# Performance work log

Hardware: AMD Instinct MI355X
Metric: run time of the kernel (lower is better)

## Reference

```python
import jax, jax.numpy as jnp
import numpy as np

B, N, D, H, L = 16, 512, 256, 8, 4
DK = D // H
EPS_LN = 1e-6
EPS_ADJ = 1e-6
NEG_INF = -1e12
LAM_ATT, LAM_DIST, LAM_ADJ = 0.3, 0.3, 0.4
SLOPE = 0.1  # leaky_relu_slope


def setup_inputs() -> dict:
    key = jax.random.key(0)
    ks = jax.random.split(key, 24)
    s = 1.0 / np.sqrt(D)
    w = lambda k: jax.random.normal(k, (L, D, D), jnp.float32) * s
    b = lambda k: jax.random.normal(k, (L, D), jnp.float32) * 0.01
    return {
        "x": jax.random.normal(ks[0], (B, N, D), jnp.float32),
        "mask": jax.random.randint(ks[1], (B, N), 0, 2, jnp.int32),
        "adj_matrix": jax.random.uniform(ks[2], (B, N, N), jnp.float32),
        "distance_matrix": jax.random.uniform(ks[3], (B, N, N), jnp.float32) * 10.0,
        "edges_att": jnp.zeros((1,), jnp.float32),  # unused (use_edge_features=False)
        "Wq": w(ks[4]), "bq": b(ks[5]),
        "Wk": w(ks[6]), "bk": b(ks[7]),
        "Wv": w(ks[8]), "bv": b(ks[9]),
        "Wo": w(ks[10]), "bo": b(ks[11]),
        "Wf1": w(ks[12]), "bf1": b(ks[13]),
        "Wf2": w(ks[14]), "bf2": b(ks[15]),
        "ln1_a": jnp.ones((L, D), jnp.float32), "ln1_b": jnp.zeros((L, D), jnp.float32),
        "ln2_a": jnp.ones((L, D), jnp.float32), "ln2_b": jnp.zeros((L, D), jnp.float32),
        "lnf_a": jnp.ones((D,), jnp.float32), "lnf_b": jnp.zeros((D,), jnp.float32),
    }


def _layernorm(x, a, b):
    # torch LayerNorm here uses unbiased std and divides by (std + eps)
    m = x.mean(-1, keepdims=True)
    s = jnp.std(x, axis=-1, ddof=1, keepdims=True)
    return a * (x - m) / (s + EPS_LN) + b


def reference(x, mask, adj_matrix, distance_matrix, edges_att,
              Wq, bq, Wk, bk, Wv, bv, Wo, bo, Wf1, bf1, Wf2, bf2,
              ln1_a, ln1_b, ln2_a, ln2_b, lnf_a, lnf_b):
    maskk = (mask != 0)[:, None, :]                      # [B,1,N] key mask
    # distance kernel: softmax(-dist) with masked keys -> weight 0
    p_dist = jax.nn.softmax(jnp.where(maskk, -distance_matrix, -jnp.inf), axis=-1)  # [B,N,N]
    # row-normalized adjacency
    p_adj = adj_matrix / (adj_matrix.sum(-1, keepdims=True) + EPS_ADJ)              # [B,N,N]
    mk4 = maskk[:, :, None, :]                           # [B,1,1,N]
    inv_sqrt_dk = 1.0 / np.sqrt(DK)

    for i in range(L):
        # --- self-attention sublayer (pre-norm residual) ---
        h_in = _layernorm(x, ln1_a[i], ln1_b[i])
        q = (h_in @ Wq[i] + bq[i]).reshape(B, N, H, DK).transpose(0, 2, 1, 3)
        k = (h_in @ Wk[i] + bk[i]).reshape(B, N, H, DK).transpose(0, 2, 1, 3)
        v = (h_in @ Wv[i] + bv[i]).reshape(B, N, H, DK).transpose(0, 2, 1, 3)
        scores = jnp.einsum('bhqd,bhkd->bhqk', q, k) * inv_sqrt_dk
        p_attn = jax.nn.softmax(jnp.where(mk4, scores, NEG_INF), axis=-1)
        # three-way fused weighting over [B,H,N,N]
        p = LAM_ATT * p_attn + LAM_DIST * p_dist[:, None] + LAM_ADJ * p_adj[:, None]
        att = jnp.einsum('bhqk,bhkd->bhqd', p, v).transpose(0, 2, 1, 3).reshape(B, N, D)
        x = x + (att @ Wo[i] + bo[i])
        # --- FFN sublayer (pre-norm residual), N_dense=2 with leaky_relu ---
        h2 = _layernorm(x, ln2_a[i], ln2_b[i])
        h2 = jax.nn.leaky_relu(h2 @ Wf1[i] + bf1[i], negative_slope=SLOPE)
        h2 = jax.nn.leaky_relu(h2 @ Wf2[i] + bf2[i], negative_slope=SLOPE)
        x = x + h2

    return _layernorm(x, lnf_a, lnf_b)
```

## Files before the change

### kernel.cpp

```cpp
#include <hip/hip_runtime.h>
#include <hip/hip_bf16.h>
#include <math.h>

constexpr int kB  = 16;
constexpr int kN  = 512;
constexpr int kD  = 256;
constexpr int kH  = 8;
constexpr int kDK = 32;
constexpr int kL  = 4;

using bf16 = __hip_bfloat16;
using short8 = __attribute__((ext_vector_type(8))) short;
using floatx4 = __attribute__((ext_vector_type(4))) float;

__device__ __forceinline__ float fast_exp2(float x) {
#if __has_builtin(__builtin_amdgcn_exp2f)
    return __builtin_amdgcn_exp2f(x);
#else
    return __expf(x * 0.69314718055994531f);
#endif
}

__device__ __forceinline__ void gl2lds16(const bf16* g, bf16* s) {
    __builtin_amdgcn_global_load_lds(
        (const __attribute__((address_space(1))) void*)g,
        (__attribute__((address_space(3))) void*)s, 16, 0, 0);
}

__device__ __forceinline__ int swzA(int row, int inrow_byte) {
    return row * 512 + (inrow_byte ^ ((row & 7) << 4));
}

__device__ __forceinline__ float blockReduceSum(float v, float* sh) {
    #pragma unroll
    for (int o = 32; o > 0; o >>= 1) v += __shfl_down(v, o, 64);
    int lane = threadIdx.x & 63, w = threadIdx.x >> 6;
    __syncthreads();
    if (lane == 0) sh[w] = v;
    __syncthreads();
    return sh[0] + sh[1] + sh[2] + sh[3];
}

__device__ __forceinline__ float blockReduceMax(float v, float* sh) {
    #pragma unroll
    for (int o = 32; o > 0; o >>= 1) v = fmaxf(v, __shfl_down(v, o, 64));
    int lane = threadIdx.x & 63, w = threadIdx.x >> 6;
    __syncthreads();
    if (lane == 0) sh[w] = v;
    __syncthreads();
    return fmaxf(fmaxf(sh[0], sh[1]), fmaxf(sh[2], sh[3]));
}

__global__ __launch_bounds__(256) void wconv_kernel(const float* __restrict__ Wq,
                                                    const float* __restrict__ Wk,
                                                    const float* __restrict__ Wv,
                                                    const float* __restrict__ Wo,
                                                    const float* __restrict__ Wf1,
                                                    const float* __restrict__ Wf2,
                                                    bf16* __restrict__ wqkv,
                                                    bf16* __restrict__ wo,
                                                    bf16* __restrict__ wf1,
                                                    bf16* __restrict__ wf2) {
    __shared__ float tile[32][33];
    int bid = blockIdx.x;
    int mat = bid >> 6;
    int t6 = bid & 63;
    int tr = t6 >> 3, tc = t6 & 7;
    int layer = mat / 6, slot = mat % 6;
    const float* src =
        slot == 0 ? Wq : slot == 1 ? Wk : slot == 2 ? Wv :
        slot == 3 ? Wo : slot == 4 ? Wf1 : Wf2;
    src += (size_t)layer * kD * kD;
    bf16* dst;
    if (slot < 3) dst = wqkv + ((size_t)layer * 768 + slot * 256) * kD;
    else dst = (slot == 3 ? wo : slot == 4 ? wf1 : wf2) + (size_t)layer * kD * kD;
    int t = threadIdx.x;
    int r = t >> 5, c = t & 31;
    #pragma unroll
    for (int i = 0; i < 4; i++)
        tile[r + i * 8][c] = src[(size_t)(tr * 32 + r + i * 8) * kD + tc * 32 + c];
    __syncthreads();
    #pragma unroll
    for (int i = 0; i < 4; i++)
        dst[(size_t)(tc * 32 + r + i * 8) * kD + tr * 32 + c] = bf16(tile[c][r + i * 8]);
}

__global__ __launch_bounds__(256) void bcat_kernel(const float* __restrict__ bq,
                                                   const float* __restrict__ bk,
                                                   const float* __restrict__ bv,
                                                   float* __restrict__ bcat) {
    int idx = blockIdx.x * 256 + threadIdx.x;
    int layer = idx / 768, j = idx % 768;
    const float* s = j < 256 ? bq : j < 512 ? bk : bv;
    bcat[idx] = s[layer * 256 + (j & 255)];
}

__global__ __launch_bounds__(256) void pc_kernel(const float* __restrict__ adj,
                                                 const float* __restrict__ dist,
                                                 const int* __restrict__ mask,
                                                 bf16* __restrict__ pcb) {
    __shared__ float sh[4];
    int row = blockIdx.x;
    int b = row >> 9;
    int t = threadIdx.x;
    const float* dr = dist + (size_t)row * kN;
    const float* ar = adj + (size_t)row * kN;
    const int* mr = mask + b * kN;
    float d0 = dr[t], d1 = dr[t + 256];
    float a0 = ar[t], a1 = ar[t + 256];
    int m0 = mr[t], m1 = mr[t + 256];
    const float kLog2e = 1.4426950408889634f;
    float s0 = m0 ? -d0 * kLog2e : -INFINITY;
    float s1 = m1 ? -d1 * kLog2e : -INFINITY;
    float mx = blockReduceMax(fmaxf(s0, s1), sh);
    float e0 = fast_exp2(s0 - mx);
    float e1 = fast_exp2(s1 - mx);
    float sum  = blockReduceSum(e0 + e1, sh);
    float asum = blockReduceSum(a0 + a1, sh);
    float w_d = 0.3f / sum;
    float w_a = 0.4f / (asum + 1e-6f);
    bf16* pr = pcb + (size_t)row * kN;
    pr[t]       = bf16(e0 * w_d + a0 * w_a);
    pr[t + 256] = bf16(e1 * w_d + a1 * w_a);
}

__global__ __launch_bounds__(256) void ln_kernel(const float* __restrict__ x,
                                                 const float* __restrict__ ga,
                                                 const float* __restrict__ gb,
                                                 bf16* __restrict__ y) {
    __shared__ float sh[4];
    int row = blockIdx.x, t = threadIdx.x;
    float v = x[(size_t)row * kD + t];
    float m = blockReduceSum(v, sh) * (1.0f / kD);
    float dd = v - m;
    float var = blockReduceSum(dd * dd, sh) * (1.0f / (kD - 1));
    float s = sqrtf(var);
    y[(size_t)row * kD + t] = bf16(ga[t] * dd / (s + 1e-6f) + gb[t]);
}

__global__ __launch_bounds__(256) void gemm_qkv(const bf16* __restrict__ A,
                                                const bf16* __restrict__ Wt,
                                                const float* __restrict__ bias,
                                                bf16* __restrict__ Cv) {
    __shared__ __align__(16) bf16 As[2][128][32];
    __shared__ __align__(16) bf16 Bs[2][64][32];
    int t = threadIdx.x;
    int m0 = blockIdx.x * 128, n0 = blockIdx.y * 64;
    int lane = t & 63, w = t >> 6, g = lane >> 4, li = lane & 15;
    int sr = lane >> 2;
    int sc = (lane & 3) * 8;

    const bf16* aSrc0 = A + (size_t)(m0 + w * 32 + sr) * kD + sc;
    const bf16* aSrc1 = aSrc0 + (size_t)16 * kD;
    const bf16* bSrc  = Wt + (size_t)(n0 + w * 16 + sr) * kD + sc;

    floatx4 zero = {0.f, 0.f, 0.f, 0.f};
    floatx4 acc[2][4];
    #pragma unroll
    for (int i = 0; i < 2; i++)
        #pragma unroll
        for (int j = 0; j < 4; j++) acc[i][j] = zero;

    auto stage = [&](int buf, int k0) {
        gl2lds16(aSrc0 + k0, &As[buf][w * 32][0]);
        gl2lds16(aSrc1 + k0, &As[buf][w * 32 + 16][0]);
        gl2lds16(bSrc  + k0, &Bs[buf][w * 16][0]);
    };

    stage(0, 0);
    __syncthreads();

    #pragma unroll
    for (int ks = 0; ks < 8; ks++) {
        const int cur = ks & 1;
        if (ks < 7) stage(cur ^ 1, (ks + 1) * 32);
        short8 af0 = *(const short8*)&As[cur][w * 32 + li][g * 8];
        short8 af1 = *(const short8*)&As[cur][w * 32 + 16 + li][g * 8];
        #pragma unroll
        for (int ct = 0; ct < 4; ct++) {
            short8 bfr = *(const short8*)&Bs[cur][ct * 16 + li][g * 8];
            acc[0][ct] = __builtin_amdgcn_mfma_f32_16x16x32_bf16(af0, bfr, acc[0][ct], 0, 0, 0);
            acc[1][ct] = __builtin_amdgcn_mfma_f32_16x16x32_bf16(af1, bfr, acc[1][ct], 0, 0, 0);
        }
        if (ks < 7) __syncthreads();
    }

    #pragma unroll
    for (int rt = 0; rt < 2; rt++) {
        #pragma unroll
        for (int ct = 0; ct < 4; ct++) {
            #pragma unroll
            for (int rr = 0; rr < 4; rr++) {
                int m = m0 + w * 32 + rt * 16 + g * 4 + rr;
                int n = n0 + ct * 16 + li;
                float v = acc[rt][ct][rr] + bias[n];
                int j = n >> 8, nn = n & 255;
                int b = m >> 9, nr = m & 511;
                int hh = nn >> 5, dk = nn & 31;
                Cv[(size_t)j * (kB * kN * kD) +
                   (((size_t)(b * kH + hh)) * kN + nr) * kDK + dk] = bf16(v);
            }
        }
    }
}

__device__ __forceinline__ void gemm_phase32(const char* asb, const bf16* __restrict__ Wt,
                                             bf16 (*Bs)[256][32],
                                             int w, int lane, int g, int li,
                                             floatx4 acc[2][4]) {
    auto stageB = [&](int buf, int k0) {
        #pragma unroll
        for (int c = 0; c < 4; c++) {
            int row = w * 64 + c * 16;
            gl2lds16(Wt + (size_t)(row + (lane >> 2)) * kD + k0 + (lane & 3) * 8,
                     &Bs[buf][row][0]);
        }
    };
    stageB(0, 0);
    __syncthreads();
    #pragma unroll
    for (int ks = 0; ks < 8; ks++) {
        const int cur = ks & 1;
        if (ks < 7) stageB(cur ^ 1, (ks + 1) * 32);
        short8 af0 = *(const short8*)(asb + swzA(li,      (ks * 4 + g) << 4));
        short8 af1 = *(const short8*)(asb + swzA(li + 16, (ks * 4 + g) << 4));
        #pragma unroll
        for (int ct = 0; ct < 4; ct++) {
            short8 bfr = *(const short8*)&Bs[cur][w * 64 + ct * 16 + li][g * 8];
            acc[0][ct] = __builtin_amdgcn_mfma_f32_16x16x32_bf16(af0, bfr, acc[0][ct], 0, 0, 0);
            acc[1][ct] = __builtin_amdgcn_mfma_f32_16x16x32_bf16(af1, bfr, acc[1][ct], 0, 0, 0);
        }
        if (ks < 7) __syncthreads();
    }
}

__device__ __forceinline__ void row_ln_stats(floatx4 xv[2][4],
                                             float (*psumS)[32], float (*psqS)[32],
                                             int w, int g, int li,
                                             float outMean[2][4], float outInv[2][4]) {
    #pragma unroll
    for (int rt = 0; rt < 2; rt++) {
        #pragma unroll
        for (int rr = 0; rr < 4; rr++) {
            float s4 = 0.f, q4 = 0.f;
            #pragma unroll
            for (int ct = 0; ct < 4; ct++) {
                float v = xv[rt][ct][rr];
                s4 += v;
                q4 += v * v;
            }
            #pragma unroll
            for (int o = 1; o < 16; o <<= 1) {
                s4 += __shfl_xor(s4, o, 64);
                q4 += __shfl_xor(q4, o, 64);
            }
            int row = rt * 16 + g * 4 + rr;
            if (li == 0) { psumS[w][row] = s4; psqS[w][row] = q4; }
        }
    }
    __syncthreads();
    #pragma unroll
    for (int rt = 0; rt < 2; rt++) {
        #pragma unroll
        for (int rr = 0; rr < 4; rr++) {
            int row = rt * 16 + g * 4 + rr;
            float s  = psumS[0][row] + psumS[1][row] + psumS[2][row] + psumS[3][row];
            float ss = psqS[0][row]  + psqS[1][row]  + psqS[2][row]  + psqS[3][row];
            float mean = s * (1.0f / kD);
            float var = (ss - (float)kD * mean * mean) * (1.0f / (kD - 1));
            outMean[rt][rr] = mean;
            outInv[rt][rr] = 1.0f / (sqrtf(var) + 1e-6f);
        }
    }
}

__global__ __launch_bounds__(256) void oproj_ln(const bf16* __restrict__ A,
                                                const bf16* __restrict__ Wt,
                                                const float* __restrict__ bias,
                                                const float* __restrict__ resid,
                                                float* __restrict__ xcOut,
                                                bf16* __restrict__ hOut,
                                                const float* __restrict__ ga,
                                                const float* __restrict__ gb) {
    __shared__ __align__(16) bf16 As[32][256];
    __shared__ __align__(16) bf16 Bs[2][256][32];
    __shared__ float psumS[4][32], psqS[4][32];

    int t = threadIdx.x;
    int m0 = blockIdx.x * 32;
    int lane = t & 63, w = t >> 6, g = lane >> 4, li = lane & 15;

    {
        int r = t >> 3;
        int cbase = (t & 7) * 4;
        const bf16* src = A + (size_t)(m0 + r) * kD;
        char* asb = (char*)&As[0][0];
        #pragma unroll
        for (int c = 0; c < 4; c++) {
            int chunk = cbase + c;
            short8 v = *(const short8*)(src + chunk * 8);
            *(short8*)(asb + swzA(r, chunk << 4)) = v;
        }
    }

    floatx4 zero = {0.f, 0.f, 0.f, 0.f};
    floatx4 acc[2][4];
    #pragma unroll
    for (int i = 0; i < 2; i++)
        #pragma unroll
        for (int j = 0; j < 4; j++) acc[i][j] = zero;

    gemm_phase32((const char*)&As[0][0], Wt, Bs, w, lane, g, li, acc);

    #pragma unroll
    for (int rt = 0; rt < 2; rt++) {
        #pragma unroll
        for (int ct = 0; ct < 4; ct++) {
            #pragma unroll
            for (int rr = 0; rr < 4; rr++) {
                int m = m0 + rt * 16 + g * 4 + rr;
                int n = w * 64 + ct * 16 + li;
                float xv = resid[(size_t)m * kD + n] + acc[rt][ct][rr] + bias[n];
                xcOut[(size_t)m * kD + n] = xv;
                acc[rt][ct][rr] = xv;
            }
        }
    }

    float mean[2][4], inv[2][4];
    row_ln_stats(acc, psumS, psqS, w, g, li, mean, inv);

    #pragma unroll
    for (int rt = 0; rt < 2; rt++) {
        #pragma unroll
        for (int ct = 0; ct < 4; ct++) {
            #pragma unroll
            for (int rr = 0; rr < 4; rr++) {
                int m = m0 + rt * 16 + g * 4 + rr;
                int n = w * 64 + ct * 16 + li;
                float y = ga[n] * (acc[rt][ct][rr] - mean[rt][rr]) * inv[rt][rr] + gb[n];
                hOut[(size_t)m * kD + n] = bf16(y);
            }
        }
    }
}

template <bool LAST>
__global__ __launch_bounds__(256) void ffn_fused(const bf16* __restrict__ A,
                                                 const bf16* __restrict__ W1t,
                                                 const float* __restrict__ b1,
                                                 const bf16* __restrict__ W2t,
                                                 const float* __restrict__ b2,
                                                 const float* __restrict__ resid,
                                                 float* __restrict__ xcOut,
                                                 bf16* __restrict__ hOut,
                                                 float* __restrict__ fOut,
                                                 const float* __restrict__ ga,
                                                 const float* __restrict__ gb) {
    __shared__ __align__(16) bf16 As[32][256];
    __shared__ __align__(16) bf16 As2[32][256];
    __shared__ __align__(16) bf16 Bs[2][256][32];
    __shared__ float psumS[4][32], psqS[4][32];

    int t = threadIdx.x;
    int m0 = blockIdx.x * 32;
    int lane = t & 63, w = t >> 6, g = lane >> 4, li = lane & 15;

    {
        int r = t >> 3;
        int cbase = (t & 7) * 4;
        const bf16* src = A + (size_t)(m0 + r) * kD;
        char* asb = (char*)&As[0][0];
        #pragma unroll
        for (int c = 0; c < 4; c++) {
            int chunk = cbase + c;
            short8 v = *(const short8*)(src + chunk * 8);
            *(short8*)(asb + swzA(r, chunk << 4)) = v;
        }
    }

    floatx4 zero = {0.f, 0.f, 0.f, 0.f};
    floatx4 acc[2][4];
    #pragma unroll
    for (int i = 0; i < 2; i++)
        #pragma unroll
        for (int j = 0; j < 4; j++) acc[i][j] = zero;

    gemm_phase32((const char*)&As[0][0], W1t, Bs, w, lane, g, li, acc);

    {
        char* as2b = (char*)&As2[0][0];
        #pragma unroll
        for (int rt = 0; rt < 2; rt++) {
            #pragma unroll
            for (int ct = 0; ct < 4; ct++) {
                #pragma unroll
                for (int rr = 0; rr < 4; rr++) {
                    int row = rt * 16 + g * 4 + rr;
                    int col = w * 64 + ct * 16 + li;
                    float v = acc[rt][ct][rr] + b1[col];
                    v = v > 0.f ? v : 0.1f * v;
                    *(bf16*)(as2b + swzA(row, col * 2)) = bf16(v);
                }
            }
        }
    }
    __syncthreads();

    #pragma unroll
    for (int i = 0; i < 2; i++)
        #pragma unroll
        for (int j = 0; j < 4; j++) acc[i][j] = zero;

    gemm_phase32((const char*)&As2[0][0], W2t, Bs, w, lane, g, li, acc);

    #pragma unroll
    for (int rt = 0; rt < 2; rt++) {
        #pragma unroll
        for (int ct = 0; ct < 4; ct++) {
            #pragma unroll
            for (int rr = 0; rr < 4; rr++) {
                int m = m0 + rt * 16 + g * 4 + rr;
                int n = w * 64 + ct * 16 + li;
                float v = acc[rt][ct][rr] + b2[n];
                v = v > 0.f ? v : 0.1f * v;
                float xv = resid[(size_t)m * kD + n] + v;
                if (!LAST) xcOut[(size_t)m * kD + n] = xv;
                acc[rt][ct][rr] = xv;
            }
        }
    }

    float mean[2][4], inv[2][4];
    row_ln_stats(acc, psumS, psqS, w, g, li, mean, inv);

    #pragma unroll
    for (int rt = 0; rt < 2; rt++) {
        #pragma unroll
        for (int ct = 0; ct < 4; ct++) {
            #pragma unroll
            for (int rr = 0; rr < 4; rr++) {
                int m = m0 + rt * 16 + g * 4 + rr;
                int n = w * 64 + ct * 16 + li;
                float y = ga[n] * (acc[rt][ct][rr] - mean[rt][rr]) * inv[rt][rr] + gb[n];
                if (LAST) fOut[(size_t)m * kD + n] = y;
                else      hOut[(size_t)m * kD + n] = bf16(y);
            }
        }
    }
}

__global__ __launch_bounds__(256, 2) void attn_mfma(const bf16* __restrict__ qb,
                                                    const bf16* __restrict__ kb,
                                                    const bf16* __restrict__ vb,
                                                    const bf16* __restrict__ pcb,
                                                    const int* __restrict__ mask,
                                                    bf16* __restrict__ att) {
    __shared__ __align__(16) bf16 Vf[16 * 2 * 64 * 8];
    __shared__ __align__(16) bf16 Pbuf[4][16][136];

    int blk = blockIdx.x;
    int qt = blk & 7;
    int bh = blk >> 3;
    int b = bh >> 3;
    int h = bh & 7;
    int t = threadIdx.x;
    int lane = t & 63, w = t >> 6;
    int g = lane >> 4, li = lane & 15;

    {
        const float4* vsrc4 = (const float4*)(vb + (size_t)bh * kN * kDK);
        #pragma unroll
        for (int it = 0; it < 8; it++) {
            int idx = t + it * 256;
            float4 raw = vsrc4[idx];
            union { float4 f; bf16 hh[8]; } u; u.f = raw;
            int f0 = idx * 8;
            int n = f0 >> 5, dk0 = f0 & 31;
            int kt = n >> 5, j = n & 7, gsl = (n >> 3) & 3;
            #pragma unroll
            for (int e = 0; e < 8; e++) {
                int dk = dk0 + e;
                int dt = dk >> 4;
                int lsl = (gsl << 4) | (dk & 15);
                Vf[((((kt << 1) | dt) << 6) | lsl) * 8 + j] = u.hh[e];
            }
        }
    }
    __syncthreads();

    const bf16* qrow = qb + ((size_t)bh * kN + qt * 64 + w * 16 + li) * kDK + g * 8;
    short8 aQ = *(const short8*)qrow;
    const bf16* kbase = kb + (size_t)bh * kN * kDK;
    const int* mb = mask + b * kN;
    unsigned mbits = 0;
    #pragma unroll
    for (int tt = 0; tt < 32; tt++)
        mbits |= (unsigned)(mb[tt * 16 + li] != 0) << tt;

    floatx4 s[32];
    floatx4 zero = {0.f, 0.f, 0.f, 0.f};
    #pragma unroll
    for (int tt = 0; tt < 32; tt++) {
        short8 bK = *(const short8*)(kbase + (size_t)(tt * 16 + li) * kDK + g * 8);
        s[tt] = __builtin_amdgcn_mfma_f32_16x16x32_bf16(aQ, bK, zero, 0, 0, 0);
    }

    const float scale = 0.17677669529663689f * 1.4426950408889634f;
    #pragma unroll
    for (int tt = 0; tt < 32; tt++) {
        bool mm = (mbits >> tt) & 1;
        #pragma unroll
        for (int r = 0; r < 4; r++)
            s[tt][r] = mm ? s[tt][r] * scale : -1e12f;
    }

    #pragma unroll
    for (int r = 0; r < 4; r++) {
        float mx = s[0][r];
        #pragma unroll
        for (int tt = 1; tt < 32; tt++) mx = fmaxf(mx, s[tt][r]);
        #pragma unroll
        for (int o = 1; o < 16; o <<= 1) mx = fmaxf(mx, __shfl_xor(mx, o, 64));
        float sum = 0.f;
        #pragma unroll
        for (int tt = 0; tt < 32; tt++) {
            float e = fast_exp2(s[tt][r] - mx);
            s[tt][r] = e;
            sum += e;
        }
        #pragma unroll
        for (int o = 1; o < 16; o <<= 1) sum += __shfl_xor(sum, o, 64);
        float inv = 0.3f / sum;
        #pragma unroll
        for (int tt = 0; tt < 32; tt++) s[tt][r] *= inv;
    }

    bf16* pb = &Pbuf[w][0][0];
    const bf16* pcrow = pcb + ((size_t)b * kN + qt * 64 + w * 16) * kN;
    floatx4 accA0 = zero, accA1 = zero, accB0 = zero, accB1 = zero;
    #pragma unroll
    for (int c = 0; c < 4; c++) {
        #pragma unroll
        for (int ttl = 0; ttl < 8; ttl++) {
            int tt = c * 8 + ttl;
            int kcol = ttl * 16 + li;
            #pragma unroll
            for (int r = 0; r < 4; r++)
                pb[(g * 4 + r) * 136 + kcol] = bf16(s[tt][r]);
        }
        #pragma unroll
        for (int k2 = 0; k2 < 4; k2++) {
            int ktile = c * 4 + k2;
            short8 aP = *(const short8*)(pb + li * 136 + k2 * 32 + g * 8);
            short8 aC = *(const short8*)(pcrow + (size_t)li * kN + c * 128 + k2 * 32 + g * 8);
            short8 bV0 = *(const short8*)(&Vf[((ktile * 2 + 0) * 64 + lane) * 8]);
            short8 bV1 = *(const short8*)(&Vf[((ktile * 2 + 1) * 64 + lane) * 8]);
            accA0 = __builtin_amdgcn_mfma_f32_16x16x32_bf16(aP, bV0, accA0, 0, 0, 0);
            accA1 = __builtin_amdgcn_mfma_f32_16x16x32_bf16(aP, bV1, accA1, 0, 0, 0);
            accB0 = __builtin_amdgcn_mfma_f32_16x16x32_bf16(aC, bV0, accB0, 0, 0, 0);
            accB1 = __builtin_amdgcn_mfma_f32_16x16x32_bf16(aC, bV1, accB1, 0, 0, 0);
        }
    }

    #pragma unroll
    for (int r = 0; r < 4; r++) {
        size_t row = (size_t)b * kN + qt * 64 + w * 16 + g * 4 + r;
        bf16* arow = att + row * kD + h * kDK;
        arow[li]      = bf16(accA0[r] + accB0[r]);
        arow[16 + li] = bf16(accA1[r] + accB1[r]);
    }
}

extern "C" void kernel_launch(void* const* d_in, const int* in_sizes, int n_in,
                              void* d_out, int out_size, void* d_ws, size_t ws_size,
                              hipStream_t stream) {
    const float* x    = (const float*)d_in[0];
    const int*   mask = (const int*)d_in[1];
    const float* adj  = (const float*)d_in[2];
    const float* dist = (const float*)d_in[3];
    const float* Wq = (const float*)d_in[5];  const float* bq = (const float*)d_in[6];
    const float* Wk = (const float*)d_in[7];  const float* bk = (const float*)d_in[8];
    const float* Wv = (const float*)d_in[9];  const float* bv = (const float*)d_in[10];
    const float* Wo = (const float*)d_in[11]; const float* bo = (const float*)d_in[12];
    const float* Wf1 = (const float*)d_in[13]; const float* bf1 = (const float*)d_in[14];
    const float* Wf2 = (const float*)d_in[15]; const float* bf2 = (const float*)d_in[16];
    const float* ln1a = (const float*)d_in[17]; const float* ln1b = (const float*)d_in[18];
    const float* ln2a = (const float*)d_in[19]; const float* ln2b = (const float*)d_in[20];
    const float* lnfa = (const float*)d_in[21]; const float* lnfb = (const float*)d_in[22];

    const size_t rows = (size_t)kB * kN;
    const size_t actN = rows * kD;

    char* wsb = (char*)d_ws;
    bf16*  pcb   = (bf16*)wsb;  wsb += (size_t)kB * kN * kN * sizeof(bf16);
    float* xc    = (float*)wsb; wsb += actN * sizeof(float);
    bf16*  h     = (bf16*)wsb;  wsb += actN * sizeof(bf16);
    bf16*  attb  = (bf16*)wsb;  wsb += actN * sizeof(bf16);
    bf16*  qkvb  = (bf16*)wsb;  wsb += 3 * actN * sizeof(bf16);
    bf16*  wqkv  = (bf16*)wsb;  wsb += (size_t)kL * 768 * kD * sizeof(bf16);
    bf16*  wo_t  = (bf16*)wsb;  wsb += (size_t)kL * kD * kD * sizeof(bf16);
    bf16*  wf1_t = (bf16*)wsb;  wsb += (size_t)kL * kD * kD * sizeof(bf16);
    bf16*  wf2_t = (bf16*)wsb;  wsb += (size_t)kL * kD * kD * sizeof(bf16);
    float* bcat  = (float*)wsb; wsb += (size_t)kL * 768 * sizeof(float);

    wconv_kernel<<<24 * 64, 256, 0, stream>>>(Wq, Wk, Wv, Wo, Wf1, Wf2, wqkv, wo_t, wf1_t, wf2_t);
    bcat_kernel<<<kL * 768 / 256, 256, 0, stream>>>(bq, bk, bv, bcat);
    pc_kernel<<<kB * kN, 256, 0, stream>>>(adj, dist, mask, pcb);
    ln_kernel<<<rows, 256, 0, stream>>>(x, ln1a, ln1b, h);

    dim3 gQKV(64, 12);
    const int g32 = rows / 32;
    for (int i = 0; i < kL; i++) {
        const size_t bOff = (size_t)i * kD;
        const size_t wOff = (size_t)i * kD * kD;
        const float* xin = (i == 0) ? x : xc;
        gemm_qkv<<<gQKV, 256, 0, stream>>>(h, wqkv + (size_t)i * 768 * kD,
                                           bcat + (size_t)i * 768, qkvb);
        attn_mfma<<<kB * kH * (kN / 64), 256, 0, stream>>>(qkvb, qkvb + actN, qkvb + 2 * actN,
                                                           pcb, mask, attb);
        oproj_ln<<<g32, 256, 0, stream>>>(attb, wo_t + wOff, bo + bOff, xin,
                                          xc, h, ln2a + bOff, ln2b + bOff);
        if (i < kL - 1) {
            ffn_fused<false><<<g32, 256, 0, stream>>>(h, wf1_t + wOff, bf1 + bOff,
                                                      wf2_t + wOff, bf2 + bOff,
                                                      xc, xc, h, nullptr,
                                                      ln1a + (size_t)(i + 1) * kD,
                                                      ln1b + (size_t)(i + 1) * kD);
        } else {
            ffn_fused<true><<<g32, 256, 0, stream>>>(h, wf1_t + wOff, bf1 + bOff,
                                                     wf2_t + wOff, bf2 + bOff,
                                                     xc, nullptr, nullptr, (float*)d_out,
                                                     lnfa, lnfb);
        }
    }
}
```

Baseline: 396.1 us.

## Share head-independent pc@V product across heads and store V transposed

The combined distance/adjacency weight matrix is the same for every head, so its product with V is now computed once per batch as a [N,N]x[N,D] GEMM in extra blocks of the attention launch, instead of once per head inside each attention block. The QKV GEMM now writes V in a transposed per-head layout, so the attention blocks read it straight from global memory and drop the LDS V reshuffle. The two partial attention outputs are summed in bf16 when o-proj loads its input, which adds one more activation buffer read and an extra rounding step.

Result: slower. 476.4 us (+20.3%).

```diff
diff --git a/kernel.cpp b/kernel.cpp
--- a/kernel.cpp
+++ b/kernel.cpp
@@ -19,6 +19,15 @@
 #else
     return __expf(x * 0.69314718055994531f);
 #endif
+}
+
+__device__ __forceinline__ float bfs2f(short s) {
+    unsigned u = ((unsigned)(unsigned short)s) << 16;
+    return __uint_as_float(u);
+}
+__device__ __forceinline__ short f2bfs(float f) {
+    bf16 b(f);
+    return *reinterpret_cast<short*>(&b);
 }
 
 __device__ __forceinline__ void gl2lds16(const bf16* g, bf16* s) {
@@ -197,10 +206,171 @@
                 int j = n >> 8, nn = n & 255;
                 int b = m >> 9, nr = m & 511;
                 int hh = nn >> 5, dk = nn & 31;
-                Cv[(size_t)j * (kB * kN * kD) +
-                   (((size_t)(b * kH + hh)) * kN + nr) * kDK + dk] = bf16(v);
-            }
-        }
+                size_t off = (size_t)j * (kB * kN * kD);
+                if (j < 2)
+                    Cv[off + (((size_t)(b * kH + hh)) * kN + nr) * kDK + dk] = bf16(v);
+                else
+                    Cv[off + (((size_t)(b * kH + hh)) * kDK + dk) * kN + nr] = bf16(v);
+            }
+        }
+    }
+}
+
+struct SmGemm { bf16 As[2][128][32]; bf16 Bs[2][64][32]; };
+struct SmAttn { bf16 P[4][16][136]; };
+union SmU { SmGemm g; SmAttn a; };
+
+__global__ __launch_bounds__(256) void attn_pc(const bf16* __restrict__ qb,
+                                               const bf16* __restrict__ kb,
+                                               const bf16* __restrict__ vtb,
+                                               const bf16* __restrict__ pcb,
+                                               const int* __restrict__ mask,
+                                               bf16* __restrict__ att,
+                                               bf16* __restrict__ attpc) {
+    __shared__ __align__(16) SmU sm;
+    int t = threadIdx.x;
+    int lane = t & 63, w = t >> 6;
+    int g = lane >> 4, li = lane & 15;
+    floatx4 zero = {0.f, 0.f, 0.f, 0.f};
+
+    if (blockIdx.x >= 1024) {
+        int idx = blockIdx.x - 1024;
+        int b  = idx >> 4;
+        int mt = (idx >> 2) & 3, nt = idx & 3;
+        int m0 = mt * 128, n0 = nt * 64;
+        int sr = lane >> 2, sc = (lane & 3) * 8;
+
+        const bf16* Arows = pcb + ((size_t)b * kN) * kN;
+        const bf16* Brows = vtb + ((size_t)b * kD) * kN;
+        const bf16* aSrc0 = Arows + (size_t)(m0 + w * 32 + sr) * kN + sc;
+        const bf16* aSrc1 = aSrc0 + (size_t)16 * kN;
+        const bf16* bSrc  = Brows + (size_t)(n0 + w * 16 + sr) * kN + sc;
+
+        floatx4 acc[2][4];
+        #pragma unroll
+        for (int i = 0; i < 2; i++)
+            #pragma unroll
+            for (int j = 0; j < 4; j++) acc[i][j] = zero;
+
+        auto stage = [&](int buf, int k0) {
+            gl2lds16(aSrc0 + k0, &sm.g.As[buf][w * 32][0]);
+            gl2lds16(aSrc1 + k0, &sm.g.As[buf][w * 32 + 16][0]);
+            gl2lds16(bSrc  + k0, &sm.g.Bs[buf][w * 16][0]);
+        };
+        stage(0, 0);
+        __syncthreads();
+        #pragma unroll
+        for (int ks = 0; ks < 16; ks++) {
+            const int cur = ks & 1;
+            if (ks < 15) stage(cur ^ 1, (ks + 1) * 32);
+            short8 af0 = *(const short8*)&sm.g.As[cur][w * 32 + li][g * 8];
+            short8 af1 = *(const short8*)&sm.g.As[cur][w * 32 + 16 + li][g * 8];
+            #pragma unroll
+            for (int ct = 0; ct < 4; ct++) {
+                short8 bfr = *(const short8*)&sm.g.Bs[cur][ct * 16 + li][g * 8];
+                acc[0][ct] = __builtin_amdgcn_mfma_f32_16x16x32_bf16(af0, bfr, acc[0][ct], 0, 0, 0);
+                acc[1][ct] = __builtin_amdgcn_mfma_f32_16x16x32_bf16(af1, bfr, acc[1][ct], 0, 0, 0);
+            }
+            if (ks < 15) __syncthreads();
+        }
+        #pragma unroll
+        for (int rt = 0; rt < 2; rt++) {
+            #pragma unroll
+            for (int ct = 0; ct < 4; ct++) {
+                #pragma unroll
+                for (int rr = 0; rr < 4; rr++) {
+                    int m = m0 + w * 32 + rt * 16 + g * 4 + rr;
+                    int n = n0 + ct * 16 + li;
+                    attpc[((size_t)b * kN + m) * kD + n] = bf16(acc[rt][ct][rr]);
+                }
+            }
+        }
+        return;
+    }
+
+    int blk = blockIdx.x;
+    int qt = blk & 7;
+    int bh = blk >> 3;
+    int b = bh >> 3;
+    int h = bh & 7;
+
+    const bf16* qrow = qb + ((size_t)bh * kN + qt * 64 + w * 16 + li) * kDK + g * 8;
+    short8 aQ = *(const short8*)qrow;
+    const bf16* kbase = kb + (size_t)bh * kN * kDK;
+    const int* mb = mask + b * kN;
+    unsigned mbits = 0;
+    #pragma unroll
+    for (int tt = 0; tt < 32; tt++)
+        mbits |= (unsigned)(mb[tt * 16 + li] != 0) << tt;
+
+    floatx4 s[32];
+    #pragma unroll
+    for (int tt = 0; tt < 32; tt++) {
+        short8 bK = *(const short8*)(kbase + (size_t)(tt * 16 + li) * kDK + g * 8);
+        s[tt] = __builtin_amdgcn_mfma_f32_16x16x32_bf16(aQ, bK, zero, 0, 0, 0);
+    }
+
+    const float scale = 0.17677669529663689f * 1.4426950408889634f;
+    #pragma unroll
+    for (int tt = 0; tt < 32; tt++) {
+        bool mm = (mbits >> tt) & 1;
+        #pragma unroll
+        for (int r = 0; r < 4; r++)
+            s[tt][r] = mm ? s[tt][r] * scale : -1e12f;
+    }
+
+    #pragma unroll
+    for (int r = 0; r < 4; r++) {
+        float mx = s[0][r];
+        #pragma unroll
+        for (int tt = 1; tt < 32; tt++) mx = fmaxf(mx, s[tt][r]);
+        #pragma unroll
+        for (int o = 1; o < 16; o <<= 1) mx = fmaxf(mx, __shfl_xor(mx, o, 64));
+        float sum = 0.f;
+        #pragma unroll
+        for (int tt = 0; tt < 32; tt++) {
+            float e = fast_exp2(s[tt][r] - mx);
+            s[tt][r] = e;
+            sum += e;
+        }
+        #pragma unroll
+        for (int o = 1; o < 16; o <<= 1) sum += __shfl_xor(sum, o, 64);
+        float inv = 0.3f / sum;
+        #pragma unroll
+        for (int tt = 0; tt < 32; tt++) s[tt][r] *= inv;
+    }
+
+    bf16* pb = &sm.a.P[w][0][0];
+    const bf16* vrow0 = vtb + ((size_t)bh * kDK + li) * kN;
+    const bf16* vrow1 = vrow0 + (size_t)16 * kN;
+    floatx4 accA0 = zero, accA1 = zero;
+    #pragma unroll
+    for (int c = 0; c < 4; c++) {
+        #pragma unroll
+        for (int ttl = 0; ttl < 8; ttl++) {
+            int tt = c * 8 + ttl;
+            int kcol = ttl * 16 + li;
+            #pragma unroll
+            for (int r = 0; r < 4; r++)
+                pb[(g * 4 + r) * 136 + kcol] = bf16(s[tt][r]);
+        }
+        #pragma unroll
+        for (int k2 = 0; k2 < 4; k2++) {
+            int ktile = c * 4 + k2;
+            short8 aP  = *(const short8*)(pb + li * 136 + k2 * 32 + g * 8);
+            short8 bV0 = *(const short8*)(vrow0 + ktile * 32 + g * 8);
+            short8 bV1 = *(const short8*)(vrow1 + ktile * 32 + g * 8);
+            accA0 = __builtin_amdgcn_mfma_f32_16x16x32_bf16(aP, bV0, accA0, 0, 0, 0);
+            accA1 = __builtin_amdgcn_mfma_f32_16x16x32_bf16(aP, bV1, accA1, 0, 0, 0);
+        }
+    }
+
+    #pragma unroll
+    for (int r = 0; r < 4; r++) {
+        size_t row = (size_t)b * kN + qt * 64 + w * 16 + g * 4 + r;
+        bf16* arow = att + row * kD + h * kDK;
+        arow[li]      = bf16(accA0[r]);
+        arow[16 + li] = bf16(accA1[r]);
     }
 }
 
@@ -275,6 +445,7 @@
 }
 
 __global__ __launch_bounds__(256) void oproj_ln(const bf16* __restrict__ A,
+                                                const bf16* __restrict__ A2,
                                                 const bf16* __restrict__ Wt,
                                                 const float* __restrict__ bias,
                                                 const float* __restrict__ resid,
@@ -293,13 +464,18 @@
     {
         int r = t >> 3;
         int cbase = (t & 7) * 4;
-        const bf16* src = A + (size_t)(m0 + r) * kD;
+        const bf16* src  = A  + (size_t)(m0 + r) * kD;
+        const bf16* src2 = A2 + (size_t)(m0 + r) * kD;
         char* asb = (char*)&As[0][0];
         #pragma unroll
         for (int c = 0; c < 4; c++) {
             int chunk = cbase + c;
-            short8 v = *(const short8*)(src + chunk * 8);
-            *(short8*)(asb + swzA(r, chunk << 4)) = v;
+            short8 v1 = *(const short8*)(src  + chunk * 8);
+            short8 v2 = *(const short8*)(src2 + chunk * 8);
+            short8 o;
+            #pragma unroll
+            for (int e = 0; e < 8; e++) o[e] = f2bfs(bfs2f(v1[e]) + bfs2f(v2[e]));
+            *(short8*)(asb + swzA(r, chunk << 4)) = o;
         }
     }
 
@@ -450,128 +626,6 @@
     }
 }
 
-__global__ __launch_bounds__(256, 2) void attn_mfma(const bf16* __restrict__ qb,
-                                                    const bf16* __restrict__ kb,
-                                                    const bf16* __restrict__ vb,
-                                                    const bf16* __restrict__ pcb,
-                                                    const int* __restrict__ mask,
-                                                    bf16* __restrict__ att) {
-    __shared__ __align__(16) bf16 Vf[16 * 2 * 64 * 8];
-    __shared__ __align__(16) bf16 Pbuf[4][16][136];
-
-    int blk = blockIdx.x;
-    int qt = blk & 7;
-    int bh = blk >> 3;
-    int b = bh >> 3;
-    int h = bh & 7;
-    int t = threadIdx.x;
-    int lane = t & 63, w = t >> 6;
-    int g = lane >> 4, li = lane & 15;
-
-    {
-        const float4* vsrc4 = (const float4*)(vb + (size_t)bh * kN * kDK);
-        #pragma unroll
-        for (int it = 0; it < 8; it++) {
-            int idx = t + it * 256;
-            float4 raw = vsrc4[idx];
-            union { float4 f; bf16 hh[8]; } u; u.f = raw;
-            int f0 = idx * 8;
-            int n = f0 >> 5, dk0 = f0 & 31;
-            int kt = n >> 5, j = n & 7, gsl = (n >> 3) & 3;
-            #pragma unroll
-            for (int e = 0; e < 8; e++) {
-                int dk = dk0 + e;
-                int dt = dk >> 4;
-                int lsl = (gsl << 4) | (dk & 15);
-                Vf[((((kt << 1) | dt) << 6) | lsl) * 8 + j] = u.hh[e];
-            }
-        }
-    }
-    __syncthreads();
-
-    const bf16* qrow = qb + ((size_t)bh * kN + qt * 64 + w * 16 + li) * kDK + g * 8;
-    short8 aQ = *(const short8*)qrow;
-    const bf16* kbase = kb + (size_t)bh * kN * kDK;
-    const int* mb = mask + b * kN;
-    unsigned mbits = 0;
-    #pragma unroll
-    for (int tt = 0; tt < 32; tt++)
-        mbits |= (unsigned)(mb[tt * 16 + li] != 0) << tt;
-
-    floatx4 s[32];
-    floatx4 zero = {0.f, 0.f, 0.f, 0.f};
-    #pragma unroll
-    for (int tt = 0; tt < 32; tt++) {
-        short8 bK = *(const short8*)(kbase + (size_t)(tt * 16 + li) * kDK + g * 8);
-        s[tt] = __builtin_amdgcn_mfma_f32_16x16x32_bf16(aQ, bK, zero, 0, 0, 0);
-    }
-
-    const float scale = 0.17677669529663689f * 1.4426950408889634f;
-    #pragma unroll
-    for (int tt = 0; tt < 32; tt++) {
-        bool mm = (mbits >> tt) & 1;
-        #pragma unroll
-        for (int r = 0; r < 4; r++)
-            s[tt][r] = mm ? s[tt][r] * scale : -1e12f;
-    }
-
-    #pragma unroll
-    for (int r = 0; r < 4; r++) {
-        float mx = s[0][r];
-        #pragma unroll
-        for (int tt = 1; tt < 32; tt++) mx = fmaxf(mx, s[tt][r]);
-        #pragma unroll
-        for (int o = 1; o < 16; o <<= 1) mx = fmaxf(mx, __shfl_xor(mx, o, 64));
-        float sum = 0.f;
-        #pragma unroll
-        for (int tt = 0; tt < 32; tt++) {
-            float e = fast_exp2(s[tt][r] - mx);
-            s[tt][r] = e;
-            sum += e;
-        }
-        #pragma unroll
-        for (int o = 1; o < 16; o <<= 1) sum += __shfl_xor(sum, o, 64);
-        float inv = 0.3f / sum;
-        #pragma unroll
-        for (int tt = 0; tt < 32; tt++) s[tt][r] *= inv;
-    }
-
-    bf16* pb = &Pbuf[w][0][0];
-    const bf16* pcrow = pcb + ((size_t)b * kN + qt * 64 + w * 16) * kN;
-    floatx4 accA0 = zero, accA1 = zero, accB0 = zero, accB1 = zero;
-    #pragma unroll
-    for (int c = 0; c < 4; c++) {
-        #pragma unroll
-        for (int ttl = 0; ttl < 8; ttl++) {
-            int tt = c * 8 + ttl;
-            int kcol = ttl * 16 + li;
-            #pragma unroll
-            for (int r = 0; r < 4; r++)
-                pb[(g * 4 + r) * 136 + kcol] = bf16(s[tt][r]);
-        }
-        #pragma unroll
-        for (int k2 = 0; k2 < 4; k2++) {
-            int ktile = c * 4 + k2;
-            short8 aP = *(const short8*)(pb + li * 136 + k2 * 32 + g * 8);
-            short8 aC = *(const short8*)(pcrow + (size_t)li * kN + c * 128 + k2 * 32 + g * 8);
-            short8 bV0 = *(const short8*)(&Vf[((ktile * 2 + 0) * 64 + lane) * 8]);
-            short8 bV1 = *(const short8*)(&Vf[((ktile * 2 + 1) * 64 + lane) * 8]);
-            accA0 = __builtin_amdgcn_mfma_f32_16x16x32_bf16(aP, bV0, accA0, 0, 0, 0);
-            accA1 = __builtin_amdgcn_mfma_f32_16x16x32_bf16(aP, bV1, accA1, 0, 0, 0);
-            accB0 = __builtin_amdgcn_mfma_f32_16x16x32_bf16(aC, bV0, accB0, 0, 0, 0);
-            accB1 = __builtin_amdgcn_mfma_f32_16x16x32_bf16(aC, bV1, accB1, 0, 0, 0);
-        }
-    }
-
-    #pragma unroll
-    for (int r = 0; r < 4; r++) {
-        size_t row = (size_t)b * kN + qt * 64 + w * 16 + g * 4 + r;
-        bf16* arow = att + row * kD + h * kDK;
-        arow[li]      = bf16(accA0[r] + accB0[r]);
-        arow[16 + li] = bf16(accA1[r] + accB1[r]);
-    }
-}
-
 extern "C" void kernel_launch(void* const* d_in, const int* in_sizes, int n_in,
                               void* d_out, int out_size, void* d_ws, size_t ws_size,
                               hipStream_t stream) {
@@ -597,6 +651,7 @@
     float* xc    = (float*)wsb; wsb += actN * sizeof(float);
     bf16*  h     = (bf16*)wsb;  wsb += actN * sizeof(bf16);
     bf16*  attb  = (bf16*)wsb;  wsb += actN * sizeof(bf16);
+    bf16*  attb2 = (bf16*)wsb;  wsb += actN * sizeof(bf16);
     bf16*  qkvb  = (bf16*)wsb;  wsb += 3 * actN * sizeof(bf16);
     bf16*  wqkv  = (bf16*)wsb;  wsb += (size_t)kL * 768 * kD * sizeof(bf16);
     bf16*  wo_t  = (bf16*)wsb;  wsb += (size_t)kL * kD * kD * sizeof(bf16);
@@ -617,9 +672,9 @@
         const float* xin = (i == 0) ? x : xc;
         gemm_qkv<<<gQKV, 256, 0, stream>>>(h, wqkv + (size_t)i * 768 * kD,
                                            bcat + (size_t)i * 768, qkvb);
-        attn_mfma<<<kB * kH * (kN / 64), 256, 0, stream>>>(qkvb, qkvb + actN, qkvb + 2 * actN,
-                                                           pcb, mask, attb);
-        oproj_ln<<<g32, 256, 0, stream>>>(attb, wo_t + wOff, bo + bOff, xin,
+        attn_pc<<<1024 + 256, 256, 0, stream>>>(qkvb, qkvb + actN, qkvb + 2 * actN,
+                                                pcb, mask, attb, attb2);
+        oproj_ln<<<g32, 256, 0, stream>>>(attb, attb2, wo_t + wOff, bo + bOff, xin,
                                           xc, h, ln2a + bOff, ln2b + bOff);
         if (i < kL - 1) {
             ffn_fused<false><<<g32, 256, 0, stream>>>(h, wf1_t + wOff, bf1 + bOff,
```

## Write V transposed from QKV GEMM and read it directly in attention

Applied to the files above, without the earlier changes.

The QKV GEMM now stages V-column tiles through shared memory and writes V in a transposed [bh][dk][n] layout with 16-byte stores. The attention kernel drops its per-block LDS rearrangement of V and reads B-operand fragments for the PV MFMAs straight from global memory. This removes redundant V reshuffling, which was repeated for each of 8 query tiles per head, along with its LDS footprint and a barrier. The cost is extra LDS traffic and a sync in the GEMM epilogue, plus uncached global reads of V inside the attention inner loop.

Result: slower. 488.2 us (+23.2%).

```diff
diff --git a/kernel.cpp b/kernel.cpp
--- a/kernel.cpp
+++ b/kernel.cpp
@@ -142,8 +142,10 @@
                                                 const bf16* __restrict__ Wt,
                                                 const float* __restrict__ bias,
                                                 bf16* __restrict__ Cv) {
-    __shared__ __align__(16) bf16 As[2][128][32];
-    __shared__ __align__(16) bf16 Bs[2][64][32];
+    __shared__ __align__(16) union {
+        struct { bf16 As[2][128][32]; bf16 Bs[2][64][32]; } g;
+        bf16 tr[64][136];
+    } sm;
     int t = threadIdx.x;
     int m0 = blockIdx.x * 128, n0 = blockIdx.y * 64;
     int lane = t & 63, w = t >> 6, g = lane >> 4, li = lane & 15;
@@ -162,9 +164,9 @@
         for (int j = 0; j < 4; j++) acc[i][j] = zero;
 
     auto stage = [&](int buf, int k0) {
-        gl2lds16(aSrc0 + k0, &As[buf][w * 32][0]);
-        gl2lds16(aSrc1 + k0, &As[buf][w * 32 + 16][0]);
-        gl2lds16(bSrc  + k0, &Bs[buf][w * 16][0]);
+        gl2lds16(aSrc0 + k0, &sm.g.As[buf][w * 32][0]);
+        gl2lds16(aSrc1 + k0, &sm.g.As[buf][w * 32 + 16][0]);
+        gl2lds16(bSrc  + k0, &sm.g.Bs[buf][w * 16][0]);
     };
 
     stage(0, 0);
@@ -174,33 +176,165 @@
     for (int ks = 0; ks < 8; ks++) {
         const int cur = ks & 1;
         if (ks < 7) stage(cur ^ 1, (ks + 1) * 32);
-        short8 af0 = *(const short8*)&As[cur][w * 32 + li][g * 8];
-        short8 af1 = *(const short8*)&As[cur][w * 32 + 16 + li][g * 8];
+        short8 af0 = *(const short8*)&sm.g.As[cur][w * 32 + li][g * 8];
+        short8 af1 = *(const short8*)&sm.g.As[cur][w * 32 + 16 + li][g * 8];
         #pragma unroll
         for (int ct = 0; ct < 4; ct++) {
-            short8 bfr = *(const short8*)&Bs[cur][ct * 16 + li][g * 8];
+            short8 bfr = *(const short8*)&sm.g.Bs[cur][ct * 16 + li][g * 8];
             acc[0][ct] = __builtin_amdgcn_mfma_f32_16x16x32_bf16(af0, bfr, acc[0][ct], 0, 0, 0);
             acc[1][ct] = __builtin_amdgcn_mfma_f32_16x16x32_bf16(af1, bfr, acc[1][ct], 0, 0, 0);
         }
         if (ks < 7) __syncthreads();
     }
 
-    #pragma unroll
-    for (int rt = 0; rt < 2; rt++) {
-        #pragma unroll
-        for (int ct = 0; ct < 4; ct++) {
-            #pragma unroll
-            for (int rr = 0; rr < 4; rr++) {
-                int m = m0 + w * 32 + rt * 16 + g * 4 + rr;
-                int n = n0 + ct * 16 + li;
-                float v = acc[rt][ct][rr] + bias[n];
-                int j = n >> 8, nn = n & 255;
-                int b = m >> 9, nr = m & 511;
-                int hh = nn >> 5, dk = nn & 31;
-                Cv[(size_t)j * (kB * kN * kD) +
-                   (((size_t)(b * kH + hh)) * kN + nr) * kDK + dk] = bf16(v);
-            }
-        }
+    if (blockIdx.y < 8) {
+        #pragma unroll
+        for (int rt = 0; rt < 2; rt++) {
+            #pragma unroll
+            for (int ct = 0; ct < 4; ct++) {
+                #pragma unroll
+                for (int rr = 0; rr < 4; rr++) {
+                    int m = m0 + w * 32 + rt * 16 + g * 4 + rr;
+                    int n = n0 + ct * 16 + li;
+                    float v = acc[rt][ct][rr] + bias[n];
+                    int j = n >> 8, nn = n & 255;
+                    int b = m >> 9, nr = m & 511;
+                    int hh = nn >> 5, dk = nn & 31;
+                    Cv[(size_t)j * (kB * kN * kD) +
+                       (((size_t)(b * kH + hh)) * kN + nr) * kDK + dk] = bf16(v);
+                }
+            }
+        }
+    } else {
+        __syncthreads();
+        #pragma unroll
+        for (int rt = 0; rt < 2; rt++) {
+            #pragma unroll
+            for (int ct = 0; ct < 4; ct++) {
+                #pragma unroll
+                for (int rr = 0; rr < 4; rr++) {
+                    int mloc = w * 32 + rt * 16 + g * 4 + rr;
+                    int ncol = ct * 16 + li;
+                    sm.tr[ncol][mloc] = bf16(acc[rt][ct][rr] + bias[n0 + ncol]);
+                }
+            }
+        }
+        __syncthreads();
+        int b = m0 >> 9;
+        int nrbase = m0 & 511;
+        bf16* vtb = Cv + 2 * (size_t)(kB * kN * kD);
+        #pragma unroll
+        for (int it = 0; it < 4; it++) {
+            int idx = t + it * 256;
+            int rid = idx >> 4;
+            int cid = (idx & 15) * 8;
+            int nn = (n0 + rid) & 255;
+            int hh = nn >> 5, dk = nn & 31;
+            bf16* dst = vtb + (((size_t)(b * kH + hh)) * kDK + dk) * kN + nrbase + cid;
+            *(short8*)dst = *(const short8*)&sm.tr[rid][cid];
+        }
+    }
+}
+
+__global__ __launch_bounds__(256) void attn_mfma(const bf16* __restrict__ qb,
+                                                 const bf16* __restrict__ kb,
+                                                 const bf16* __restrict__ vtb,
+                                                 const bf16* __restrict__ pcb,
+                                                 const int* __restrict__ mask,
+                                                 bf16* __restrict__ att) {
+    __shared__ __align__(16) bf16 Pbuf[4][16][136];
+
+    int blk = blockIdx.x;
+    int qt = blk & 7;
+    int bh = blk >> 3;
+    int b = bh >> 3;
+    int h = bh & 7;
+    int t = threadIdx.x;
+    int lane = t & 63, w = t >> 6;
+    int g = lane >> 4, li = lane & 15;
+    floatx4 zero = {0.f, 0.f, 0.f, 0.f};
+
+    const bf16* qrow = qb + ((size_t)bh * kN + qt * 64 + w * 16 + li) * kDK + g * 8;
+    short8 aQ = *(const short8*)qrow;
+    const bf16* kbase = kb + (size_t)bh * kN * kDK;
+    const int* mb = mask + b * kN;
+    unsigned mbits = 0;
+    #pragma unroll
+    for (int tt = 0; tt < 32; tt++)
+        mbits |= (unsigned)(mb[tt * 16 + li] != 0) << tt;
+
+    floatx4 s[32];
+    #pragma unroll
+    for (int tt = 0; tt < 32; tt++) {
+        short8 bK = *(const short8*)(kbase + (size_t)(tt * 16 + li) * kDK + g * 8);
+        s[tt] = __builtin_amdgcn_mfma_f32_16x16x32_bf16(aQ, bK, zero, 0, 0, 0);
+    }
+
+    const float scale = 0.17677669529663689f * 1.4426950408889634f;
+    #pragma unroll
+    for (int tt = 0; tt < 32; tt++) {
+        bool mm = (mbits >> tt) & 1;
+        #pragma unroll
+        for (int r = 0; r < 4; r++)
+            s[tt][r] = mm ? s[tt][r] * scale : -1e12f;
+    }
+
+    #pragma unroll
+    for (int r = 0; r < 4; r++) {
+        float mx = s[0][r];
+        #pragma unroll
+        for (int tt = 1; tt < 32; tt++) mx = fmaxf(mx, s[tt][r]);
+        #pragma unroll
+        for (int o = 1; o < 16; o <<= 1) mx = fmaxf(mx, __shfl_xor(mx, o, 64));
+        float sum = 0.f;
+        #pragma unroll
+        for (int tt = 0; tt < 32; tt++) {
+            float e = fast_exp2(s[tt][r] - mx);
+            s[tt][r] = e;
+            sum += e;
+        }
+        #pragma unroll
+        for (int o = 1; o < 16; o <<= 1) sum += __shfl_xor(sum, o, 64);
+        float inv = 0.3f / sum;
+        #pragma unroll
+        for (int tt = 0; tt < 32; tt++) s[tt][r] *= inv;
+    }
+
+    bf16* pb = &Pbuf[w][0][0];
+    const bf16* pcrow = pcb + ((size_t)b * kN + qt * 64 + w * 16) * kN;
+    const bf16* vrow0 = vtb + ((size_t)bh * kDK + li) * kN;
+    const bf16* vrow1 = vrow0 + (size_t)16 * kN;
+    floatx4 accA0 = zero, accA1 = zero, accB0 = zero, accB1 = zero;
+    #pragma unroll
+    for (int c = 0; c < 4; c++) {
+        #pragma unroll
+        for (int ttl = 0; ttl < 8; ttl++) {
+            int tt = c * 8 + ttl;
+            int kcol = ttl * 16 + li;
+            #pragma unroll
+            for (int r = 0; r < 4; r++)
+                pb[(g * 4 + r) * 136 + kcol] = bf16(s[tt][r]);
+        }
+        #pragma unroll
+        for (int k2 = 0; k2 < 4; k2++) {
+            int ktile = c * 4 + k2;
+            short8 aP  = *(const short8*)(pb + li * 136 + k2 * 32 + g * 8);
+            short8 aC  = *(const short8*)(pcrow + (size_t)li * kN + c * 128 + k2 * 32 + g * 8);
+            short8 bV0 = *(const short8*)(vrow0 + ktile * 32 + g * 8);
+            short8 bV1 = *(const short8*)(vrow1 + ktile * 32 + g * 8);
+            accA0 = __builtin_amdgcn_mfma_f32_16x16x32_bf16(aP, bV0, accA0, 0, 0, 0);
+            accA1 = __builtin_amdgcn_mfma_f32_16x16x32_bf16(aP, bV1, accA1, 0, 0, 0);
+            accB0 = __builtin_amdgcn_mfma_f32_16x16x32_bf16(aC, bV0, accB0, 0, 0, 0);
+            accB1 = __builtin_amdgcn_mfma_f32_16x16x32_bf16(aC, bV1, accB1, 0, 0, 0);
+        }
+    }
+
+    #pragma unroll
+    for (int r = 0; r < 4; r++) {
+        size_t row = (size_t)b * kN + qt * 64 + w * 16 + g * 4 + r;
+        bf16* arow = att + row * kD + h * kDK;
+        arow[li]      = bf16(accA0[r] + accB0[r]);
+        arow[16 + li] = bf16(accA1[r] + accB1[r]);
     }
 }
 
@@ -450,128 +584,6 @@
     }
 }
 
-__global__ __launch_bounds__(256, 2) void attn_mfma(const bf16* __restrict__ qb,
-                                                    const bf16* __restrict__ kb,
-                                                    const bf16* __restrict__ vb,
-                                                    const bf16* __restrict__ pcb,
-                                                    const int* __restrict__ mask,
-                                                    bf16* __restrict__ att) {
-    __shared__ __align__(16) bf16 Vf[16 * 2 * 64 * 8];
-    __shared__ __align__(16) bf16 Pbuf[4][16][136];
-
-    int blk = blockIdx.x;
-    int qt = blk & 7;
-    int bh = blk >> 3;
-    int b = bh >> 3;
-    int h = bh & 7;
-    int t = threadIdx.x;
-    int lane = t & 63, w = t >> 6;
-    int g = lane >> 4, li = lane & 15;
-
-    {
-        const float4* vsrc4 = (const float4*)(vb + (size_t)bh * kN * kDK);
-        #pragma unroll
-        for (int it = 0; it < 8; it++) {
-            int idx = t + it * 256;
-            float4 raw = vsrc4[idx];
-            union { float4 f; bf16 hh[8]; } u; u.f = raw;
-            int f0 = idx * 8;
-            int n = f0 >> 5, dk0 = f0 & 31;
-            int kt = n >> 5, j = n & 7, gsl = (n >> 3) & 3;
-            #pragma unroll
-            for (int e = 0; e < 8; e++) {
-                int dk = dk0 + e;
-                int dt = dk >> 4;
-                int lsl = (gsl << 4) | (dk & 15);
-                Vf[((((kt << 1) | dt) << 6) | lsl) * 8 + j] = u.hh[e];
-            }
-        }
-    }
-    __syncthreads();
-
-    const bf16* qrow = qb + ((size_t)bh * kN + qt * 64 + w * 16 + li) * kDK + g * 8;
-    short8 aQ = *(const short8*)qrow;
-    const bf16* kbase = kb + (size_t)bh * kN * kDK;
-    const int* mb = mask + b * kN;
-    unsigned mbits = 0;
-    #pragma unroll
-    for (int tt = 0; tt < 32; tt++)
-        mbits |= (unsigned)(mb[tt * 16 + li] != 0) << tt;
-
-    floatx4 s[32];
-    floatx4 zero = {0.f, 0.f, 0.f, 0.f};
-    #pragma unroll
-    for (int tt = 0; tt < 32; tt++) {
-        short8 bK = *(const short8*)(kbase + (size_t)(tt * 16 + li) * kDK + g * 8);
-        s[tt] = __builtin_amdgcn_mfma_f32_16x16x32_bf16(aQ, bK, zero, 0, 0, 0);
-    }
-
-    const float scale = 0.17677669529663689f * 1.4426950408889634f;
-    #pragma unroll
-    for (int tt = 0; tt < 32; tt++) {
-        bool mm = (mbits >> tt) & 1;
-        #pragma unroll
-        for (int r = 0; r < 4; r++)
-            s[tt][r] = mm ? s[tt][r] * scale : -1e12f;
-    }
-
-    #pragma unroll
-    for (int r = 0; r < 4; r++) {
-        float mx = s[0][r];
-        #pragma unroll
-        for (int tt = 1; tt < 32; tt++) mx = fmaxf(mx, s[tt][r]);
-        #pragma unroll
-        for (int o = 1; o < 16; o <<= 1) mx = fmaxf(mx, __shfl_xor(mx, o, 64));
-        float sum = 0.f;
-        #pragma unroll
-        for (int tt = 0; tt < 32; tt++) {
-            float e = fast_exp2(s[tt][r] - mx);
-            s[tt][r] = e;
-            sum += e;
-        }
-        #pragma unroll
-        for (int o = 1; o < 16; o <<= 1) sum += __shfl_xor(sum, o, 64);
-        float inv = 0.3f / sum;
-        #pragma unroll
-        for (int tt = 0; tt < 32; tt++) s[tt][r] *= inv;
-    }
-
-    bf16* pb = &Pbuf[w][0][0];
-    const bf16* pcrow = pcb + ((size_t)b * kN + qt * 64 + w * 16) * kN;
-    floatx4 accA0 = zero, accA1 = zero, accB0 = zero, accB1 = zero;
-    #pragma unroll
-    for (int c = 0; c < 4; c++) {
-        #pragma unroll
-        for (int ttl = 0; ttl < 8; ttl++) {
-            int tt = c * 8 + ttl;
-            int kcol = ttl * 16 + li;
-            #pragma unroll
-            for (int r = 0; r < 4; r++)
-                pb[(g * 4 + r) * 136 + kcol] = bf16(s[tt][r]);
-        }
-        #pragma unroll
-        for (int k2 = 0; k2 < 4; k2++) {
-            int ktile = c * 4 + k2;
-            short8 aP = *(const short8*)(pb + li * 136 + k2 * 32 + g * 8);
-            short8 aC = *(const short8*)(pcrow + (size_t)li * kN + c * 128 + k2 * 32 + g * 8);
-            short8 bV0 = *(const short8*)(&Vf[((ktile * 2 + 0) * 64 + lane) * 8]);
-            short8 bV1 = *(const short8*)(&Vf[((ktile * 2 + 1) * 64 + lane) * 8]);
-            accA0 = __builtin_amdgcn_mfma_f32_16x16x32_bf16(aP, bV0, accA0, 0, 0, 0);
-            accA1 = __builtin_amdgcn_mfma_f32_16x16x32_bf16(aP, bV1, accA1, 0, 0, 0);
-            accB0 = __builtin_amdgcn_mfma_f32_16x16x32_bf16(aC, bV0, accB0, 0, 0, 0);
-            accB1 = __builtin_amdgcn_mfma_f32_16x16x32_bf16(aC, bV1, accB1, 0, 0, 0);
-        }
-    }
-
-    #pragma unroll
-    for (int r = 0; r < 4; r++) {
-        size_t row = (size_t)b * kN + qt * 64 + w * 16 + g * 4 + r;
-        bf16* arow = att + row * kD + h * kDK;
-        arow[li]      = bf16(accA0[r] + accB0[r]);
-        arow[16 + li] = bf16(accA1[r] + accB1[r]);
-    }
-}
-
 extern "C" void kernel_launch(void* const* d_in, const int* in_sizes, int n_in,
                               void* d_out, int out_size, void* d_ws, size_t ws_size,
                               hipStream_t stream) {
@@ -617,7 +629,8 @@
         const float* xin = (i == 0) ? x : xc;
         gemm_qkv<<<gQKV, 256, 0, stream>>>(h, wqkv + (size_t)i * 768 * kD,
                                            bcat + (size_t)i * 768, qkvb);
-        attn_mfma<<<kB * kH * (kN / 64), 256, 0, stream>>>(qkvb, qkvb + actN, qkvb + 2 * actN,
+        attn_mfma<<<kB * kH * (kN / 64), 256, 0, stream>>>(qkvb, qkvb + actN,
+                                                           qkvb + 2 * actN,
                                                            pcb, mask, attb);
         oproj_ln<<<g32, 256, 0, stream>>>(attb, wo_t + wOff, bo + bOff, xin,
                                           xc, h, ln2a + bOff, ln2b + bOff);
```
